# Kernel optimization log

Measured on AMD Instinct MI355X. Metric: run time of the kernel, lower is better.

## Reference

```python
import jax, jax.numpy as jnp
import numpy as np

SQ, B, H, D = 2048, 1, 16, 64
HIDDEN = H * D


def setup_inputs() -> dict:
    key = jax.random.key(0)
    kq, kk, kv = jax.random.split(key, 3)
    query_layer = jax.random.normal(kq, (SQ, B, H, D), dtype=jnp.float32)
    key_layer = jax.random.normal(kk, (SQ, B, H, D), dtype=jnp.float32)
    value_layer = jax.random.normal(kv, (SQ, B, H, D), dtype=jnp.float32)
    return {"query_layer": query_layer, "key_layer": key_layer, "value_layer": value_layer}


def reference(query_layer, key_layer, value_layer):
    sq, b, h, d = query_layer.shape
    sk = key_layer.shape[0]
    norm = 1.0 / jnp.sqrt(jnp.asarray(d, dtype=query_layer.dtype))
    # scores: [b, h, sq, sk]  (materialized in the original via baddbmm)
    scores = jnp.einsum('sbhd,tbhd->bhst', query_layer, key_layer) * norm
    # causal mask (tril over [sq, sk]); masked positions -> -10000.0 as in original
    causal = jnp.tril(jnp.ones((sq, sk), dtype=bool))
    scores = jnp.where(causal[None, None], scores, jnp.asarray(-10000.0, scores.dtype))
    probs = jax.nn.softmax(scores, axis=-1)
    # context: [sq, b, h, d] -> [sq, b, hidden]
    ctx = jnp.einsum('bhst,tbhd->sbhd', probs, value_layer)
    return ctx.reshape(sq, b, h * d)
```

## Files before the change

kernel.cpp:

```cpp
#include <hip/hip_runtime.h>

typedef __bf16 bf16_t;
typedef bf16_t bf16x4 __attribute__((ext_vector_type(4)));
typedef bf16_t bf16x8 __attribute__((ext_vector_type(8)));
typedef float f32x4 __attribute__((ext_vector_type(4)));
typedef float f32x16 __attribute__((ext_vector_type(16)));

namespace {
constexpr int kNH  = 16;
constexpr int kHD  = 64;
constexpr int kHID = kNH * kHD;
constexpr int kSQ  = 2048;
constexpr int kKP  = 72;
constexpr int kOmPitch = 68;
constexpr int kSmBytes = 71680;
constexpr int kKbElems = kNH * kSQ * kHD;
}

__global__ __launch_bounds__(256)
void prep_kernel(const float* __restrict__ Kg, const float* __restrict__ Vg,
                 bf16_t* __restrict__ Kb, bf16_t* __restrict__ Vb) {
  __shared__ bf16_t ls[32][64];
  const int bid = blockIdx.x;
  const int tid = threadIdx.x;
  if (bid < 1024) {
    const int o    = (bid * 256 + tid) * 8;
    const int head = o >> 17;
    const int t    = (o >> 6) & 2047;
    const int d0   = o & 63;
    const float4 f0 = *(const float4*)(Kg + (size_t)t * kHID + head * kHD + d0);
    const float4 f1 = *(const float4*)(Kg + (size_t)t * kHID + head * kHD + d0 + 4);
    bf16x8 hk;
    hk[0] = (bf16_t)f0.x; hk[1] = (bf16_t)f0.y; hk[2] = (bf16_t)f0.z; hk[3] = (bf16_t)f0.w;
    hk[4] = (bf16_t)f1.x; hk[5] = (bf16_t)f1.y; hk[6] = (bf16_t)f1.z; hk[7] = (bf16_t)f1.w;
    *(bf16x8*)(Kb + o) = hk;
  } else {
    const int vb   = bid - 1024;
    const int head = vb >> 6;
    const int tile = vb & 63;
    #pragma unroll
    for (int s = 0; s < 2; ++s) {
      const int idx = tid + 256 * s;
      const int row = idx >> 4;
      const int c4  = (idx & 15) * 4;
      const float4 f =
          *(const float4*)(Vg + (size_t)(tile * 32 + row) * kHID + head * kHD + c4);
      bf16x4 hv4;
      hv4[0] = (bf16_t)f.x; hv4[1] = (bf16_t)f.y;
      hv4[2] = (bf16_t)f.z; hv4[3] = (bf16_t)f.w;
      *(bf16x4*)(&ls[row][c4]) = hv4;
    }
    __syncthreads();
    const int lane = tid >> 2;
    const int hh   = lane >> 5;
    const int m31  = lane & 31;
    const int q    = tid & 3;
    const int db   = q >> 1, tp = q & 1;
    bf16x8 hv;
    #pragma unroll
    for (int j = 0; j < 8; ++j)
      hv[j] = ls[4 * hh + 16 * tp + (j & 3) + 8 * (j >> 2)][m31 + 32 * db];
    *(bf16x8*)(Vb + ((size_t)(head * 64 + tile) * 64 + lane) * 32 + (db * 16 + tp * 8)) = hv;
  }
}

__global__ __launch_bounds__(512, 2)
void fattn_kernel(const float* __restrict__ Qg, const bf16_t* __restrict__ Kb,
                  const bf16_t* __restrict__ Vb, float* __restrict__ Og) {
  __shared__ __align__(16) unsigned char smraw[kSmBytes];
  bf16_t* sm = (bf16_t*)smraw;
  bf16_t* qs = sm;

  const int bid  = blockIdx.x;
  const int head = bid & (kNH - 1);
  const int ip   = bid >> 4;

  const int tid  = threadIdx.x;
  const int wave = tid >> 6;
  const int lane = tid & 63;
  const int h    = lane >> 5;
  const int m31  = lane & 31;

  const float kQScale = 0.125f * 1.44269504088896340736f;

  const bf16_t* kfb = Kb + (size_t)head * (kSQ * kHD) + (size_t)m31 * kHD + 8 * h;
  const bf16_t* vfb = Vb + ((size_t)head * 64 * 64 + lane) * 32;

  for (int halfq = 0; halfq < 2; ++halfq) {
    const int mblk = halfq ? ip : (31 - ip);
    const int m0   = mblk * 64;
    const int mtk  = 2 * mblk + 1;

    __syncthreads();
    #pragma unroll
    for (int i = 0; i < 2; ++i) {
      const int idx = tid + 512 * i;
      const int row = idx >> 4;
      const int c4  = (idx & 15) * 4;
      const float4 f = *(const float4*)(Qg + (size_t)(m0 + row) * kHID + head * kHD + c4);
      bf16x4 qv;
      qv[0] = (bf16_t)(f.x * kQScale); qv[1] = (bf16_t)(f.y * kQScale);
      qv[2] = (bf16_t)(f.z * kQScale); qv[3] = (bf16_t)(f.w * kQScale);
      *(bf16x4*)(qs + row * kKP + c4) = qv;
    }
    __syncthreads();

    bf16x8 qf00 = *(const bf16x8*)(qs + m31 * kKP +  0 + 8 * h);
    bf16x8 qf01 = *(const bf16x8*)(qs + m31 * kKP + 16 + 8 * h);
    bf16x8 qf02 = *(const bf16x8*)(qs + m31 * kKP + 32 + 8 * h);
    bf16x8 qf03 = *(const bf16x8*)(qs + m31 * kKP + 48 + 8 * h);
    bf16x8 qf10 = *(const bf16x8*)(qs + (32 + m31) * kKP +  0 + 8 * h);
    bf16x8 qf11 = *(const bf16x8*)(qs + (32 + m31) * kKP + 16 + 8 * h);
    bf16x8 qf12 = *(const bf16x8*)(qs + (32 + m31) * kKP + 32 + 8 * h);
    bf16x8 qf13 = *(const bf16x8*)(qs + (32 + m31) * kKP + 48 + 8 * h);

    f32x16 Oa00, Oa10, Oa01, Oa11;
    #pragma unroll
    for (int r = 0; r < 16; ++r) { Oa00[r] = 0.f; Oa10[r] = 0.f; Oa01[r] = 0.f; Oa11[r] = 0.f; }
    float lacc0 = 0.f, lacc1 = 0.f;

    bf16x8 k0, k1, k2, k3, v0, v1, v2, v3;
    int jt = wave;
    if (jt <= mtk) {
      const bf16_t* kp = kfb + (size_t)jt * 2048;
      k0 = *(const bf16x8*)(kp);      k1 = *(const bf16x8*)(kp + 16);
      k2 = *(const bf16x8*)(kp + 32); k3 = *(const bf16x8*)(kp + 48);
      const bf16_t* vp = vfb + (size_t)jt * 2048;
      v0 = *(const bf16x8*)(vp);      v1 = *(const bf16x8*)(vp + 8);
      v2 = *(const bf16x8*)(vp + 16); v3 = *(const bf16x8*)(vp + 24);
    }
    for (; jt <= mtk; jt += 8) {
      const int kv0  = jt * 32;
      const bool do0 = (kv0 <= m0);

      f32x16 c0, c1;
      if (do0) {
        #pragma unroll
        for (int r = 0; r < 16; ++r) c0[r] = 0.f;
        c0 = __builtin_amdgcn_mfma_f32_32x32x16_bf16(k0, qf00, c0, 0, 0, 0);
        c0 = __builtin_amdgcn_mfma_f32_32x32x16_bf16(k1, qf01, c0, 0, 0, 0);
        c0 = __builtin_amdgcn_mfma_f32_32x32x16_bf16(k2, qf02, c0, 0, 0, 0);
        c0 = __builtin_amdgcn_mfma_f32_32x32x16_bf16(k3, qf03, c0, 0, 0, 0);
      }
      #pragma unroll
      for (int r = 0; r < 16; ++r) c1[r] = 0.f;
      c1 = __builtin_amdgcn_mfma_f32_32x32x16_bf16(k0, qf10, c1, 0, 0, 0);
      c1 = __builtin_amdgcn_mfma_f32_32x32x16_bf16(k1, qf11, c1, 0, 0, 0);
      c1 = __builtin_amdgcn_mfma_f32_32x32x16_bf16(k2, qf12, c1, 0, 0, 0);
      c1 = __builtin_amdgcn_mfma_f32_32x32x16_bf16(k3, qf13, c1, 0, 0, 0);

      if (jt + 8 <= mtk) {
        const bf16_t* kp = kfb + (size_t)(jt + 8) * 2048;
        k0 = *(const bf16x8*)(kp);      k1 = *(const bf16x8*)(kp + 16);
        k2 = *(const bf16x8*)(kp + 32); k3 = *(const bf16x8*)(kp + 48);
      }

      if (do0) {
        float p[16];
        if (kv0 == m0) {
          #pragma unroll
          for (int r = 0; r < 16; ++r) {
            const int kr = (r & 3) + 8 * (r >> 2) + 4 * h;
            const float e = __builtin_amdgcn_exp2f(c0[r]);
            p[r] = (kr <= m31) ? e : 0.f;
            lacc0 += p[r];
          }
        } else {
          #pragma unroll
          for (int r = 0; r < 16; ++r) { p[r] = __builtin_amdgcn_exp2f(c0[r]); lacc0 += p[r]; }
        }
        bf16x8 pb0, pb1;
        #pragma unroll
        for (int j = 0; j < 8; ++j) { pb0[j] = (bf16_t)p[j]; pb1[j] = (bf16_t)p[8 + j]; }
        Oa00 = __builtin_amdgcn_mfma_f32_32x32x16_bf16(v0, pb0, Oa00, 0, 0, 0);
        Oa10 = __builtin_amdgcn_mfma_f32_32x32x16_bf16(v2, pb0, Oa10, 0, 0, 0);
        Oa00 = __builtin_amdgcn_mfma_f32_32x32x16_bf16(v1, pb1, Oa00, 0, 0, 0);
        Oa10 = __builtin_amdgcn_mfma_f32_32x32x16_bf16(v3, pb1, Oa10, 0, 0, 0);
      }

      {
        float p[16];
        if (kv0 == m0 + 32) {
          #pragma unroll
          for (int r = 0; r < 16; ++r) {
            const int kr = (r & 3) + 8 * (r >> 2) + 4 * h;
            const float e = __builtin_amdgcn_exp2f(c1[r]);
            p[r] = (kr <= m31) ? e : 0.f;
            lacc1 += p[r];
          }
        } else {
          #pragma unroll
          for (int r = 0; r < 16; ++r) { p[r] = __builtin_amdgcn_exp2f(c1[r]); lacc1 += p[r]; }
        }
        bf16x8 pb0, pb1;
        #pragma unroll
        for (int j = 0; j < 8; ++j) { pb0[j] = (bf16_t)p[j]; pb1[j] = (bf16_t)p[8 + j]; }
        Oa01 = __builtin_amdgcn_mfma_f32_32x32x16_bf16(v0, pb0, Oa01, 0, 0, 0);
        Oa11 = __builtin_amdgcn_mfma_f32_32x32x16_bf16(v2, pb0, Oa11, 0, 0, 0);
        Oa01 = __builtin_amdgcn_mfma_f32_32x32x16_bf16(v1, pb1, Oa01, 0, 0, 0);
        Oa11 = __builtin_amdgcn_mfma_f32_32x32x16_bf16(v3, pb1, Oa11, 0, 0, 0);
      }

      if (jt + 8 <= mtk) {
        const bf16_t* vp = vfb + (size_t)(jt + 8) * 2048;
        v0 = *(const bf16x8*)(vp);      v1 = *(const bf16x8*)(vp + 8);
        v2 = *(const bf16x8*)(vp + 16); v3 = *(const bf16x8*)(vp + 24);
      }
    }

    float* fv   = (float*)smraw;
    float* Om   = fv + wave * 32 * kOmPitch;
    float* larr = fv + 8 * 32 * kOmPitch;

    #pragma unroll
    for (int qh = 0; qh < 2; ++qh) {
      __syncthreads();
      {
        const f32x16& A0 = qh ? Oa01 : Oa00;
        const f32x16& A1 = qh ? Oa11 : Oa10;
        #pragma unroll
        for (int q = 0; q < 4; ++q) {
          f32x4 w0, w1;
          #pragma unroll
          for (int e = 0; e < 4; ++e) { w0[e] = A0[4 * q + e]; w1[e] = A1[4 * q + e]; }
          *(f32x4*)(Om + (size_t)m31 * kOmPitch + 8 * q + 4 * h)      = w0;
          *(f32x4*)(Om + (size_t)m31 * kOmPitch + 32 + 8 * q + 4 * h) = w1;
        }
        larr[wave * 64 + lane] = qh ? lacc1 : lacc0;
      }
      __syncthreads();
      {
        const int row = tid >> 4;
        const int c4  = (tid & 15) * 4;
        float l = 0.f;
        #pragma unroll
        for (int w = 0; w < 8; ++w)
          l += larr[w * 64 + row] + larr[w * 64 + 32 + row];
        const float inv = 1.f / l;
        f32x4 o;
        #pragma unroll
        for (int e = 0; e < 4; ++e) o[e] = 0.f;
        #pragma unroll
        for (int w = 0; w < 8; ++w) {
          const f32x4 a = *(const f32x4*)(fv + w * 32 * kOmPitch + (size_t)row * kOmPitch + c4);
          #pragma unroll
          for (int e = 0; e < 4; ++e) o[e] += a[e];
        }
        #pragma unroll
        for (int e = 0; e < 4; ++e) o[e] *= inv;
        *(f32x4*)(Og + (size_t)(m0 + 32 * qh + row) * kHID + head * kHD + c4) = o;
      }
    }
  }
}

extern "C" void kernel_launch(void* const* d_in, const int* in_sizes, int n_in,
                              void* d_out, int out_size, void* d_ws, size_t ws_size,
                              hipStream_t stream) {
  (void)in_sizes; (void)n_in; (void)ws_size; (void)out_size;
  const float* Q = (const float*)d_in[0];
  const float* K = (const float*)d_in[1];
  const float* V = (const float*)d_in[2];
  float* O = (float*)d_out;
  bf16_t* Kb = (bf16_t*)d_ws;
  bf16_t* Vb = Kb + kKbElems;
  hipLaunchKernelGGL(prep_kernel, dim3(2048), dim3(256), 0, stream, K, V, Kb, Vb);
  dim3 grid(256);
  dim3 block(512);
  hipLaunchKernelGGL(fattn_kernel, grid, block, 0, stream, Q, Kb, Vb, O);
}
```

Baseline: 92.60 us.

## Fuse K/V bf16 prep into attention kernel via cooperative grid sync

Merges the separate K/V fp32-to-bf16 conversion kernel into the attention kernel. All 256 blocks do their share of the conversion, then hit a grid-wide barrier through a cooperative launch before running attention. This removes one kernel launch and the gap between the two kernels, but adds the cost of a grid sync and requires every block to be co-resident.

```diff
diff --git a/kernel.cpp b/kernel.cpp
--- a/kernel.cpp
+++ b/kernel.cpp
@@ -1,4 +1,7 @@
 #include <hip/hip_runtime.h>
+#include <hip/hip_cooperative_groups.h>
+
+namespace cg = cooperative_groups;
 
 typedef __bf16 bf16_t;
 typedef bf16_t bf16x4 __attribute__((ext_vector_type(4)));
@@ -17,65 +20,72 @@
 constexpr int kKbElems = kNH * kSQ * kHD;
 }
 
-__global__ __launch_bounds__(256)
-void prep_kernel(const float* __restrict__ Kg, const float* __restrict__ Vg,
-                 bf16_t* __restrict__ Kb, bf16_t* __restrict__ Vb) {
-  __shared__ bf16_t ls[32][64];
-  const int bid = blockIdx.x;
-  const int tid = threadIdx.x;
-  if (bid < 1024) {
-    const int o    = (bid * 256 + tid) * 8;
-    const int head = o >> 17;
-    const int t    = (o >> 6) & 2047;
-    const int d0   = o & 63;
-    const float4 f0 = *(const float4*)(Kg + (size_t)t * kHID + head * kHD + d0);
-    const float4 f1 = *(const float4*)(Kg + (size_t)t * kHID + head * kHD + d0 + 4);
-    bf16x8 hk;
-    hk[0] = (bf16_t)f0.x; hk[1] = (bf16_t)f0.y; hk[2] = (bf16_t)f0.z; hk[3] = (bf16_t)f0.w;
-    hk[4] = (bf16_t)f1.x; hk[5] = (bf16_t)f1.y; hk[6] = (bf16_t)f1.z; hk[7] = (bf16_t)f1.w;
-    *(bf16x8*)(Kb + o) = hk;
-  } else {
-    const int vb   = bid - 1024;
-    const int head = vb >> 6;
-    const int tile = vb & 63;
-    #pragma unroll
-    for (int s = 0; s < 2; ++s) {
-      const int idx = tid + 256 * s;
-      const int row = idx >> 4;
-      const int c4  = (idx & 15) * 4;
-      const float4 f =
-          *(const float4*)(Vg + (size_t)(tile * 32 + row) * kHID + head * kHD + c4);
-      bf16x4 hv4;
-      hv4[0] = (bf16_t)f.x; hv4[1] = (bf16_t)f.y;
-      hv4[2] = (bf16_t)f.z; hv4[3] = (bf16_t)f.w;
-      *(bf16x4*)(&ls[row][c4]) = hv4;
-    }
-    __syncthreads();
-    const int lane = tid >> 2;
-    const int hh   = lane >> 5;
-    const int m31  = lane & 31;
-    const int q    = tid & 3;
-    const int db   = q >> 1, tp = q & 1;
-    bf16x8 hv;
-    #pragma unroll
-    for (int j = 0; j < 8; ++j)
-      hv[j] = ls[4 * hh + 16 * tp + (j & 3) + 8 * (j >> 2)][m31 + 32 * db];
-    *(bf16x8*)(Vb + ((size_t)(head * 64 + tile) * 64 + lane) * 32 + (db * 16 + tp * 8)) = hv;
+__global__ __launch_bounds__(512, 2)
+void fused_kernel(const float* __restrict__ Qg, const float* __restrict__ Kg,
+                  const float* __restrict__ Vg, bf16_t* __restrict__ Kb,
+                  bf16_t* __restrict__ Vb, float* __restrict__ Og) {
+  __shared__ __align__(16) unsigned char smraw[kSmBytes];
+
+  const int bid  = blockIdx.x;
+  const int tid  = threadIdx.x;
+
+  {
+    const int gtid = bid * 512 + tid;
+    #pragma unroll
+    for (int i = 0; i < 2; ++i) {
+      const int o    = (gtid + i * 131072) * 8;
+      const int head = o >> 17;
+      const int t    = (o >> 6) & 2047;
+      const int d0   = o & 63;
+      const float4 f0 = *(const float4*)(Kg + (size_t)t * kHID + head * kHD + d0);
+      const float4 f1 = *(const float4*)(Kg + (size_t)t * kHID + head * kHD + d0 + 4);
+      bf16x8 hk;
+      hk[0] = (bf16_t)f0.x; hk[1] = (bf16_t)f0.y; hk[2] = (bf16_t)f0.z; hk[3] = (bf16_t)f0.w;
+      hk[4] = (bf16_t)f1.x; hk[5] = (bf16_t)f1.y; hk[6] = (bf16_t)f1.z; hk[7] = (bf16_t)f1.w;
+      *(bf16x8*)(Kb + o) = hk;
+    }
+    bf16_t (*ls)[32][64] = (bf16_t (*)[32][64])smraw;
+    const int sub = tid >> 8;
+    const int t8  = tid & 255;
+    #pragma unroll
+    for (int it = 0; it < 2; ++it) {
+      const int vb   = bid * 4 + it * 2 + sub;
+      const int head = vb >> 6;
+      const int tile = vb & 63;
+      __syncthreads();
+      #pragma unroll
+      for (int s = 0; s < 2; ++s) {
+        const int idx = t8 + 256 * s;
+        const int row = idx >> 4;
+        const int c4  = (idx & 15) * 4;
+        const float4 f =
+            *(const float4*)(Vg + (size_t)(tile * 32 + row) * kHID + head * kHD + c4);
+        bf16x4 hv4;
+        hv4[0] = (bf16_t)f.x; hv4[1] = (bf16_t)f.y;
+        hv4[2] = (bf16_t)f.z; hv4[3] = (bf16_t)f.w;
+        *(bf16x4*)(&ls[sub][row][c4]) = hv4;
+      }
+      __syncthreads();
+      const int lane = t8 >> 2;
+      const int hh   = lane >> 5;
+      const int m31v = lane & 31;
+      const int q    = t8 & 3;
+      const int db   = q >> 1, tp = q & 1;
+      bf16x8 hv;
+      #pragma unroll
+      for (int j = 0; j < 8; ++j)
+        hv[j] = ls[sub][4 * hh + 16 * tp + (j & 3) + 8 * (j >> 2)][m31v + 32 * db];
+      *(bf16x8*)(Vb + ((size_t)(head * 64 + tile) * 64 + lane) * 32 + (db * 16 + tp * 8)) = hv;
+    }
   }
-}
-
-__global__ __launch_bounds__(512, 2)
-void fattn_kernel(const float* __restrict__ Qg, const bf16_t* __restrict__ Kb,
-                  const bf16_t* __restrict__ Vb, float* __restrict__ Og) {
-  __shared__ __align__(16) unsigned char smraw[kSmBytes];
-  bf16_t* sm = (bf16_t*)smraw;
-  bf16_t* qs = sm;
-
-  const int bid  = blockIdx.x;
+  __threadfence();
+  cg::this_grid().sync();
+
+  bf16_t* qs = (bf16_t*)smraw;
+
   const int head = bid & (kNH - 1);
   const int ip   = bid >> 4;
 
-  const int tid  = threadIdx.x;
   const int wave = tid >> 6;
   const int lane = tid & 63;
   const int h    = lane >> 5;
@@ -264,8 +274,7 @@
   float* O = (float*)d_out;
   bf16_t* Kb = (bf16_t*)d_ws;
   bf16_t* Vb = Kb + kKbElems;
-  hipLaunchKernelGGL(prep_kernel, dim3(2048), dim3(256), 0, stream, K, V, Kb, Vb);
-  dim3 grid(256);
-  dim3 block(512);
-  hipLaunchKernelGGL(fattn_kernel, grid, block, 0, stream, Q, Kb, Vb, O);
+  void* args[] = {(void*)&Q, (void*)&K, (void*)&V, (void*)&Kb, (void*)&Vb, (void*)&O};
+  hipLaunchCooperativeKernel((const void*)fused_kernel, dim3(256), dim3(512),
+                             args, 0, stream);
 }
```

After: 167.2 us. 80.6% more time.

## Fuse K bf16 conversion into attention kernel and shrink V prep grid

Applied to the files above, without the earlier changes.

Drops the separate K-to-bf16 pre-pass and has the attention kernel load fp32 K straight from global memory, converting to bf16 in registers just before the MFMAs. The V prep kernel now handles four tiles per block on a 256-block grid. This removes the K conversion writes and reads to the workspace, but the attention kernel now fetches twice the K bytes with strided fp32 loads and loses the next-tile K prefetch, so load latency is more exposed.

```diff
diff --git a/kernel.cpp b/kernel.cpp
--- a/kernel.cpp
+++ b/kernel.cpp
@@ -14,30 +14,18 @@
 constexpr int kKP  = 72;
 constexpr int kOmPitch = 68;
 constexpr int kSmBytes = 71680;
-constexpr int kKbElems = kNH * kSQ * kHD;
 }
 
 __global__ __launch_bounds__(256)
-void prep_kernel(const float* __restrict__ Kg, const float* __restrict__ Vg,
-                 bf16_t* __restrict__ Kb, bf16_t* __restrict__ Vb) {
+void prep_v(const float* __restrict__ Vg, bf16_t* __restrict__ Vb) {
   __shared__ bf16_t ls[32][64];
-  const int bid = blockIdx.x;
   const int tid = threadIdx.x;
-  if (bid < 1024) {
-    const int o    = (bid * 256 + tid) * 8;
-    const int head = o >> 17;
-    const int t    = (o >> 6) & 2047;
-    const int d0   = o & 63;
-    const float4 f0 = *(const float4*)(Kg + (size_t)t * kHID + head * kHD + d0);
-    const float4 f1 = *(const float4*)(Kg + (size_t)t * kHID + head * kHD + d0 + 4);
-    bf16x8 hk;
-    hk[0] = (bf16_t)f0.x; hk[1] = (bf16_t)f0.y; hk[2] = (bf16_t)f0.z; hk[3] = (bf16_t)f0.w;
-    hk[4] = (bf16_t)f1.x; hk[5] = (bf16_t)f1.y; hk[6] = (bf16_t)f1.z; hk[7] = (bf16_t)f1.w;
-    *(bf16x8*)(Kb + o) = hk;
-  } else {
-    const int vb   = bid - 1024;
+  #pragma unroll 1
+  for (int it = 0; it < 4; ++it) {
+    const int vb   = blockIdx.x * 4 + it;
     const int head = vb >> 6;
     const int tile = vb & 63;
+    if (it) __syncthreads();
     #pragma unroll
     for (int s = 0; s < 2; ++s) {
       const int idx = tid + 256 * s;
@@ -65,7 +53,7 @@
 }
 
 __global__ __launch_bounds__(512, 2)
-void fattn_kernel(const float* __restrict__ Qg, const bf16_t* __restrict__ Kb,
+void fattn_kernel(const float* __restrict__ Qg, const float* __restrict__ Kg,
                   const bf16_t* __restrict__ Vb, float* __restrict__ Og) {
   __shared__ __align__(16) unsigned char smraw[kSmBytes];
   bf16_t* sm = (bf16_t*)smraw;
@@ -83,7 +71,7 @@
 
   const float kQScale = 0.125f * 1.44269504088896340736f;
 
-  const bf16_t* kfb = Kb + (size_t)head * (kSQ * kHD) + (size_t)m31 * kHD + 8 * h;
+  const float*  kgb = Kg + (size_t)m31 * kHID + head * kHD + 8 * h;
   const bf16_t* vfb = Vb + ((size_t)head * 64 * 64 + lane) * 32;
 
   for (int halfq = 0; halfq < 2; ++halfq) {
@@ -119,12 +107,9 @@
     for (int r = 0; r < 16; ++r) { Oa00[r] = 0.f; Oa10[r] = 0.f; Oa01[r] = 0.f; Oa11[r] = 0.f; }
     float lacc0 = 0.f, lacc1 = 0.f;
 
-    bf16x8 k0, k1, k2, k3, v0, v1, v2, v3;
+    bf16x8 v0, v1, v2, v3;
     int jt = wave;
     if (jt <= mtk) {
-      const bf16_t* kp = kfb + (size_t)jt * 2048;
-      k0 = *(const bf16x8*)(kp);      k1 = *(const bf16x8*)(kp + 16);
-      k2 = *(const bf16x8*)(kp + 32); k3 = *(const bf16x8*)(kp + 48);
       const bf16_t* vp = vfb + (size_t)jt * 2048;
       v0 = *(const bf16x8*)(vp);      v1 = *(const bf16x8*)(vp + 8);
       v2 = *(const bf16x8*)(vp + 16); v3 = *(const bf16x8*)(vp + 24);
@@ -132,6 +117,25 @@
     for (; jt <= mtk; jt += 8) {
       const int kv0  = jt * 32;
       const bool do0 = (kv0 <= m0);
+
+      const float* kp = kgb + (size_t)kv0 * kHID;
+      const float4 ka0 = *(const float4*)(kp +  0);
+      const float4 kb0 = *(const float4*)(kp +  4);
+      const float4 ka1 = *(const float4*)(kp + 16);
+      const float4 kb1 = *(const float4*)(kp + 20);
+      const float4 ka2 = *(const float4*)(kp + 32);
+      const float4 kb2 = *(const float4*)(kp + 36);
+      const float4 ka3 = *(const float4*)(kp + 48);
+      const float4 kb3 = *(const float4*)(kp + 52);
+      bf16x8 k0, k1, k2, k3;
+      k0[0]=(bf16_t)ka0.x; k0[1]=(bf16_t)ka0.y; k0[2]=(bf16_t)ka0.z; k0[3]=(bf16_t)ka0.w;
+      k0[4]=(bf16_t)kb0.x; k0[5]=(bf16_t)kb0.y; k0[6]=(bf16_t)kb0.z; k0[7]=(bf16_t)kb0.w;
+      k1[0]=(bf16_t)ka1.x; k1[1]=(bf16_t)ka1.y; k1[2]=(bf16_t)ka1.z; k1[3]=(bf16_t)ka1.w;
+      k1[4]=(bf16_t)kb1.x; k1[5]=(bf16_t)kb1.y; k1[6]=(bf16_t)kb1.z; k1[7]=(bf16_t)kb1.w;
+      k2[0]=(bf16_t)ka2.x; k2[1]=(bf16_t)ka2.y; k2[2]=(bf16_t)ka2.z; k2[3]=(bf16_t)ka2.w;
+      k2[4]=(bf16_t)kb2.x; k2[5]=(bf16_t)kb2.y; k2[6]=(bf16_t)kb2.z; k2[7]=(bf16_t)kb2.w;
+      k3[0]=(bf16_t)ka3.x; k3[1]=(bf16_t)ka3.y; k3[2]=(bf16_t)ka3.z; k3[3]=(bf16_t)ka3.w;
+      k3[4]=(bf16_t)kb3.x; k3[5]=(bf16_t)kb3.y; k3[6]=(bf16_t)kb3.z; k3[7]=(bf16_t)kb3.w;
 
       f32x16 c0, c1;
       if (do0) {
@@ -148,12 +152,6 @@
       c1 = __builtin_amdgcn_mfma_f32_32x32x16_bf16(k1, qf11, c1, 0, 0, 0);
       c1 = __builtin_amdgcn_mfma_f32_32x32x16_bf16(k2, qf12, c1, 0, 0, 0);
       c1 = __builtin_amdgcn_mfma_f32_32x32x16_bf16(k3, qf13, c1, 0, 0, 0);
-
-      if (jt + 8 <= mtk) {
-        const bf16_t* kp = kfb + (size_t)(jt + 8) * 2048;
-        k0 = *(const bf16x8*)(kp);      k1 = *(const bf16x8*)(kp + 16);
-        k2 = *(const bf16x8*)(kp + 32); k3 = *(const bf16x8*)(kp + 48);
-      }
 
       if (do0) {
         float p[16];
@@ -262,10 +260,9 @@
   const float* K = (const float*)d_in[1];
   const float* V = (const float*)d_in[2];
   float* O = (float*)d_out;
-  bf16_t* Kb = (bf16_t*)d_ws;
-  bf16_t* Vb = Kb + kKbElems;
-  hipLaunchKernelGGL(prep_kernel, dim3(2048), dim3(256), 0, stream, K, V, Kb, Vb);
+  bf16_t* Vb = (bf16_t*)d_ws;
+  hipLaunchKernelGGL(prep_v, dim3(256), dim3(256), 0, stream, V, Vb);
   dim3 grid(256);
   dim3 block(512);
-  hipLaunchKernelGGL(fattn_kernel, grid, block, 0, stream, Q, Kb, Vb, O);
-}
+  hipLaunchKernelGGL(fattn_kernel, grid, block, 0, stream, Q, K, Vb, O);
+}
```

After: 99.72 us. 1.08x slower.
